# Kernel optimization log

Measured on AMD Instinct MI355X. Metric: run time of the kernel, lower is better.

Reference implementation:

```python
import jax, jax.numpy as jnp
import numpy as np

B, S, D = 2, 2048, 1024
H, HD = 16, 64  # n_heads, head_dim


def setup_inputs() -> dict:
    key = jax.random.key(0)
    ks = jax.random.split(key, 6)
    scale = 1.0 / np.sqrt(D)
    return {
        "Q": jax.random.normal(ks[0], (B, S, D), dtype=jnp.float32),
        "K": jax.random.normal(ks[1], (B, S, D), dtype=jnp.float32),
        "V": jax.random.normal(ks[2], (B, S, D), dtype=jnp.float32),
        "Wq": jax.random.normal(ks[3], (H, D, HD), dtype=jnp.float32) * scale,
        "Wv": jax.random.normal(ks[4], (H, D, HD), dtype=jnp.float32) * scale,
        "Wo": jax.random.normal(ks[5], (D, D), dtype=jnp.float32) * scale,
        "bo": jnp.zeros((D,), dtype=jnp.float32),
    }


def reference(Q, K, V, Wq, Wv, Wo, bo):
    # NOTE: original code projects K with the *query* weight (bug kept for fidelity).
    q = jnp.einsum("bsd,hdk->bhsk", Q, Wq)   # [B,H,S,HD]
    k = jnp.einsum("bsd,hdk->bhsk", K, Wq)   # query weights, per original
    v = jnp.einsum("bsd,hdk->bhsk", V, Wv)
    scores = jnp.einsum("bhsk,bhtk->bhst", q, k) / jnp.sqrt(jnp.asarray(HD, q.dtype))
    weights = jax.nn.softmax(scores, axis=-1)  # [B,H,S,S]
    attn = jnp.einsum("bhst,bhtk->bhsk", weights, v)  # [B,H,S,HD]
    concat = attn.transpose(0, 2, 1, 3).reshape(Q.shape[0], Q.shape[1], H * HD)
    return concat @ Wo.T + bo
```

## Files before the change

kernel.cpp:

```cpp
#include <hip/hip_runtime.h>

typedef __attribute__((ext_vector_type(8))) short short8;
typedef __attribute__((ext_vector_type(4))) short short4v;
typedef __attribute__((ext_vector_type(4))) float f32x4;
typedef __attribute__((ext_vector_type(16))) float f32x16;

__device__ __forceinline__ unsigned short f2bf(float f) {
  union { float f; unsigned u; } v; v.f = f;
  unsigned u = v.u;
  unsigned r = (u + 0x7FFFu + ((u >> 16) & 1u)) >> 16;
  return (unsigned short)r;
}

__device__ __forceinline__ unsigned cvtpk(float lo, float hi) {
  unsigned r;
  asm("v_cvt_pk_bf16_f32 %0, %1, %2" : "=v"(r) : "v"(lo), "v"(hi));
  return r;
}

#if __has_builtin(__builtin_amdgcn_exp2f)
__device__ __forceinline__ float exp2_fast(float x) { return __builtin_amdgcn_exp2f(x); }
#else
__device__ __forceinline__ float exp2_fast(float x) { return __expf(x * 0.69314718056f); }
#endif

__device__ __forceinline__ void gl16(const void* g, void* l) {
  __builtin_amdgcn_global_load_lds(
      (const __attribute__((address_space(1))) unsigned int*)g,
      (__attribute__((address_space(3))) unsigned int*)l, 16, 0, 0);
}

#define QSCALE 0.1803368801111f

__global__ __launch_bounds__(256)
void prep_k(const float* __restrict__ Wq, const float* __restrict__ Wv,
            const float* __restrict__ Wo, unsigned short* __restrict__ BqT,
            unsigned short* __restrict__ BvT, unsigned short* __restrict__ BoT) {
  __shared__ float tile[64 * 65];
  const int bidx = blockIdx.x;
  const int tid = threadIdx.x;
  if (bidx < 512) {
    const float* W = (bidx < 256) ? Wq : Wv;
    unsigned short* Bt = (bidx < 256) ? BqT : BvT;
    const int bb = bidx & 255;
    const int h  = bb >> 4;
    const int d0 = (bb & 15) * 64;
#pragma unroll
    for (int i = 0; i < 16; ++i) {
      int e = i * 256 + tid;
      int r = e >> 6, c = e & 63;
      tile[r * 65 + c] = W[(size_t)h * 65536 + (size_t)(d0 + r) * 64 + c];
    }
    __syncthreads();
#pragma unroll
    for (int i = 0; i < 16; ++i) {
      int e = i * 256 + tid;
      int jj = e >> 6, dd = e & 63;
      Bt[(size_t)(h * 64 + jj) * 1024 + d0 + dd] = f2bf(tile[dd * 65 + jj]);
    }
  } else {
    size_t t = (size_t)(bidx - 512) * 256 + tid;
    float4 f = *(const float4*)(Wo + t * 4);
    short4v v;
    v[0] = (short)f2bf(f.x); v[1] = (short)f2bf(f.y);
    v[2] = (short)f2bf(f.z); v[3] = (short)f2bf(f.w);
    *(short4v*)((short*)BoT + t * 4) = v;
  }
}

__global__ __launch_bounds__(256)
void conv3_k(const float* __restrict__ Q, const float* __restrict__ K,
             const float* __restrict__ V, unsigned short* __restrict__ dst) {
  const int bidx = blockIdx.x;
  const int sec = bidx >> 11;
  const float* src = (sec == 0) ? Q : (sec == 1) ? K : V;
  const float scale = (sec == 0) ? QSCALE : 1.0f;
  size_t t = (size_t)(bidx & 2047) * 256 + threadIdx.x;
  const float* s = src + t * 8;
  float4 f0 = *(const float4*)s;
  float4 f1 = *(const float4*)(s + 4);
  short8 v;
  v[0] = (short)f2bf(f0.x * scale); v[1] = (short)f2bf(f0.y * scale);
  v[2] = (short)f2bf(f0.z * scale); v[3] = (short)f2bf(f0.w * scale);
  v[4] = (short)f2bf(f1.x * scale); v[5] = (short)f2bf(f1.y * scale);
  v[6] = (short)f2bf(f1.z * scale); v[7] = (short)f2bf(f1.w * scale);
  *(short8*)(dst + (size_t)sec * 4194304 + t * 8) = v;
}

template<int EPI>
__global__ __launch_bounds__(256, 2)
void gemm3_k(const unsigned short* __restrict__ A, const unsigned short* __restrict__ Bt,
             void* __restrict__ Cp, const float* __restrict__ bias) {
  __shared__ __attribute__((aligned(16))) unsigned short As[2][64 * 64];
  __shared__ __attribute__((aligned(16))) unsigned short Bs[2][128 * 64];
  const int tid = threadIdx.x;
  const int l = tid & 63;
  const int w = tid >> 6;
  const int wr = w >> 1, wc = w & 1;
  const int lg = l >> 4, lc = l & 15;
  const int nwg = (int)gridDim.x;
  const int bid = blockIdx.x;
  const int swz = (bid & 7) * (nwg >> 3) + (bid >> 3);
  const int bm = swz >> 3, bn = swz & 7;

  const int sr = tid >> 3, ss = tid & 7;
  const unsigned short* Asrc = A  + (size_t)(bm * 64  + sr) * 1024 + ((ss ^ (sr & 7)) * 8);
  const unsigned short* Bsrc = Bt + (size_t)(bn * 128 + sr) * 1024 + ((ss ^ (sr & 7)) * 8);

  f32x4 acc[2][4] = {};

  auto stage = [&](int bufn, int k0) {
    char* ad = (char*)&As[bufn][0] + tid * 16;
    char* bd = (char*)&Bs[bufn][0] + tid * 16;
    gl16(Asrc + k0,          ad);
    gl16(Asrc + 32768 + k0,  ad + 4096);
    gl16(Bsrc + k0,          bd);
    gl16(Bsrc + 32768 + k0,  bd + 4096);
    gl16(Bsrc + 65536 + k0,  bd + 8192);
    gl16(Bsrc + 98304 + k0,  bd + 12288);
  };

  stage(0, 0);
  __syncthreads();

  int buf = 0;
  for (int it = 0; it < 16; ++it) {
    if (it < 15) stage(buf ^ 1, (it + 1) * 64);
    const unsigned short* Ac = &As[buf][0];
    const unsigned short* Bc = &Bs[buf][0];
    short8 af[2][2], bf[4][2];
#pragma unroll
    for (int mi = 0; mi < 2; ++mi)
#pragma unroll
      for (int ks = 0; ks < 2; ++ks)
        af[mi][ks] = *(const short8*)&Ac[(wr * 32 + mi * 16 + lc) * 64 + (((ks * 4 + lg) ^ (lc & 7)) * 8)];
#pragma unroll
    for (int ni = 0; ni < 4; ++ni)
#pragma unroll
      for (int ks = 0; ks < 2; ++ks)
        bf[ni][ks] = *(const short8*)&Bc[(wc * 64 + ni * 16 + lc) * 64 + (((ks * 4 + lg) ^ (lc & 7)) * 8)];
#pragma unroll
    for (int mi = 0; mi < 2; ++mi)
#pragma unroll
      for (int ni = 0; ni < 4; ++ni) {
        acc[mi][ni] = __builtin_amdgcn_mfma_f32_16x16x32_bf16(af[mi][0], bf[ni][0], acc[mi][ni], 0, 0, 0);
        acc[mi][ni] = __builtin_amdgcn_mfma_f32_16x16x32_bf16(af[mi][1], bf[ni][1], acc[mi][ni], 0, 0, 0);
      }
    __syncthreads();
    buf ^= 1;
  }

  const int m0 = bm * 64 + wr * 32 + lg * 4;
  const int n0 = bn * 128 + wc * 64 + lc;
#pragma unroll
  for (int mi = 0; mi < 2; ++mi) {
#pragma unroll
    for (int ni = 0; ni < 4; ++ni) {
      if (EPI == 1) {
        int m = m0 + mi * 16;
        int bb = m >> 11, s = m & 2047;
        int n = n0 + ni * 16;
        int hh = n >> 6, hd = n & 63;
        short4v pk;
#pragma unroll
        for (int j = 0; j < 4; ++j) pk[j] = (short)f2bf(acc[mi][ni][j]);
        *(short4v*)((unsigned short*)Cp + (size_t)((bb * 16 + hh) * 64 + hd) * 2048 + s) = pk;
      } else {
#pragma unroll
        for (int j = 0; j < 4; ++j) {
          int m = m0 + mi * 16 + j;
          int n = n0 + ni * 16;
          if (EPI == 2) ((float*)Cp)[(size_t)m * 1024 + n] = acc[mi][ni][j] + bias[n];
          else          ((unsigned short*)Cp)[(size_t)m * 1024 + n] = f2bf(acc[mi][ni][j]);
        }
      }
    }
  }
}

#define PACK8(SV, B0, W)                                                   \
  {                                                                        \
    float e0 = exp2_fast(SV[B0 + 0] - m_r), e1 = exp2_fast(SV[B0 + 1] - m_r); \
    float e2 = exp2_fast(SV[B0 + 2] - m_r), e3 = exp2_fast(SV[B0 + 3] - m_r); \
    float e4 = exp2_fast(SV[B0 + 4] - m_r), e5 = exp2_fast(SV[B0 + 5] - m_r); \
    float e6 = exp2_fast(SV[B0 + 6] - m_r), e7 = exp2_fast(SV[B0 + 7] - m_r); \
    l_r += ((e0 + e1) + (e2 + e3)) + ((e4 + e5) + (e6 + e7));              \
    unsigned Wa = cvtpk(e0, e1), Wb = cvtpk(e2, e3);                       \
    unsigned Wc = cvtpk(e4, e5), Wd = cvtpk(e6, e7);                       \
    unsigned pWa = __shfl_xor((int)Wa, 32), pWb = __shfl_xor((int)Wb, 32); \
    unsigned pWc = __shfl_xor((int)Wc, 32), pWd = __shfl_xor((int)Wd, 32); \
    W.x = hi ? pWc : Wa; W.y = hi ? pWd : Wb;                              \
    W.z = hi ? Wc : pWa; W.w = hi ? Wd : pWb;                              \
  }

#define MAX4(V, I) fmaxf(fmaxf(V[I], V[I + 1]), fmaxf(V[I + 2], V[I + 3]))

__global__ __launch_bounds__(256, 2)
void attn_k(const unsigned short* __restrict__ qh, const unsigned short* __restrict__ kh,
            const unsigned short* __restrict__ vT, unsigned short* __restrict__ attnc) {
  __shared__ __attribute__((aligned(16))) short Kb[2][4096];
  __shared__ __attribute__((aligned(16))) short Vb[2][4096];

  const int bid = (blockIdx.x & 7) * 64 + (blockIdx.x >> 3);
  const int qt = bid & 15;
  const int h = (bid >> 4) & 15;
  const int b = bid >> 8;
  const int tid = threadIdx.x;
  const int l = tid & 63;
  const int w = tid >> 6;
  const int q = l & 31;
  const int hi = l >> 5;
  const int ax = l & 7;

  const unsigned short* qb  = qh + (size_t)(b * 2048) * 1024 + h * 64;
  const unsigned short* kbf = kh + (size_t)(b * 2048) * 1024 + h * 64;
  const unsigned short* vb  = vT + (size_t)((b * 16 + h) * 64) * 2048;

  const int sr = tid >> 3, ss = tid & 7;
  const unsigned short* Ksrc = kbf + (size_t)sr * 1024 + ((ss ^ (sr & 7)) * 8);
  const unsigned short* Vsrc = vb  + (size_t)sr * 2048 + ((ss ^ (sr & 7)) * 8);

  const int s0 = qt * 128 + w * 32;
  short8 qf[4];
#pragma unroll
  for (int c = 0; c < 4; ++c)
    qf[c] = *(const short8*)(qb + (size_t)(s0 + q) * 1024 + c * 16 + hi * 8);

  float m_r = -1e30f, l_r = 0.f;
  f32x16 acc0 = {}, acc1 = {};
  const f32x16 zero16 = {};

  auto stageKV = [&](int bufn, int t0) {
    char* kd = (char*)&Kb[bufn][0] + tid * 16;
    char* vd = (char*)&Vb[bufn][0] + tid * 16;
    const unsigned short* ks = Ksrc + (size_t)t0 * 1024;
    const unsigned short* vs = Vsrc + t0;
    gl16(ks,         kd);
    gl16(ks + 32768, kd + 4096);
    gl16(vs,         vd);
    gl16(vs + 65536, vd + 4096);
  };

  stageKV(0, 0);
  __syncthreads();

  int cur = 0;
  for (int i = 0; i < 32; ++i) {
    if (i < 31) stageKV(cur ^ 1, (i + 1) * 64);

    const short* Kc = &Kb[cur][0];
    f32x16 sv0 = zero16, sv1 = zero16;
#pragma unroll
    for (int c = 0; c < 4; ++c) {
      const int gofs = (((c * 2 + hi) ^ ax) * 8);
      short8 kf0 = *(const short8*)&Kc[(q) * 64 + gofs];
      short8 kf1 = *(const short8*)&Kc[(32 + q) * 64 + gofs];
      sv0 = __builtin_amdgcn_mfma_f32_32x32x16_bf16(kf0, qf[c], sv0, 0, 0, 0);
      sv1 = __builtin_amdgcn_mfma_f32_32x32x16_bf16(kf1, qf[c], sv1, 0, 0, 0);
    }

    float tA = fmaxf(fmaxf(MAX4(sv0, 0), MAX4(sv0, 4)), fmaxf(MAX4(sv0, 8), MAX4(sv0, 12)));
    float tB = fmaxf(fmaxf(MAX4(sv1, 0), MAX4(sv1, 4)), fmaxf(MAX4(sv1, 8), MAX4(sv1, 12)));
    float tm = fmaxf(tA, tB);

    if (!__all(tm - m_r <= 8.0f)) {
      tm = fmaxf(tm, __shfl_xor(tm, 32));
      float mn = fmaxf(m_r, tm);
      float sc = exp2_fast(m_r - mn);
      m_r = mn;
      l_r *= sc;
#pragma unroll
      for (int j = 0; j < 16; ++j) { acc0[j] *= sc; acc1[j] *= sc; }
    }

    uint4 w0, w1, w2, w3;
    PACK8(sv0, 0, w0);
    PACK8(sv0, 8, w1);
    PACK8(sv1, 0, w2);
    PACK8(sv1, 8, w3);
    short8 pf0 = *reinterpret_cast<short8*>(&w0);
    short8 pf1 = *reinterpret_cast<short8*>(&w1);
    short8 pf2 = *reinterpret_cast<short8*>(&w2);
    short8 pf3 = *reinterpret_cast<short8*>(&w3);

    const short* Vc = &Vb[cur][0];
#pragma unroll
    for (int kc = 0; kc < 4; ++kc) {
      const int gofs = (((kc * 2 + hi) ^ ax) * 8);
      short8 vf0 = *(const short8*)&Vc[(q) * 64 + gofs];
      short8 vf1 = *(const short8*)&Vc[(32 + q) * 64 + gofs];
      short8 pf = (kc == 0) ? pf0 : (kc == 1) ? pf1 : (kc == 2) ? pf2 : pf3;
      acc0 = __builtin_amdgcn_mfma_f32_32x32x16_bf16(vf0, pf, acc0, 0, 0, 0);
      acc1 = __builtin_amdgcn_mfma_f32_32x32x16_bf16(vf1, pf, acc1, 0, 0, 0);
    }

    __syncthreads();
    cur ^= 1;
  }

  l_r += __shfl_xor(l_r, 32);
  float inv = 1.0f / l_r;

  unsigned short* outp = attnc + (size_t)(b * 2048 + s0 + q) * 1024 + h * 64;
#pragma unroll
  for (int t = 0; t < 4; ++t) {
    short4v p0, p1;
#pragma unroll
    for (int n = 0; n < 4; ++n) {
      p0[n] = (short)f2bf(acc0[t * 4 + n] * inv);
      p1[n] = (short)f2bf(acc1[t * 4 + n] * inv);
    }
    *(short4v*)(outp + (t * 8 + 4 * hi))      = p0;
    *(short4v*)(outp + (32 + t * 8 + 4 * hi)) = p1;
  }
}

extern "C" void kernel_launch(void* const* d_in, const int* in_sizes, int n_in,
                              void* d_out, int out_size, void* d_ws, size_t ws_size,
                              hipStream_t stream) {
  const float* Q  = (const float*)d_in[0];
  const float* Kt = (const float*)d_in[1];
  const float* V  = (const float*)d_in[2];
  const float* Wq = (const float*)d_in[3];
  const float* Wv = (const float*)d_in[4];
  const float* Wo = (const float*)d_in[5];
  const float* bo = (const float*)d_in[6];
  float* out = (float*)d_out;

  char* ws = (char*)d_ws;
  unsigned short* QKb  = (unsigned short*)(ws);
  unsigned short* Vb   = (unsigned short*)(ws + ((size_t)16 << 20));
  unsigned short* qh   = (unsigned short*)(ws + ((size_t)24 << 20));
  unsigned short* BqT  = (unsigned short*)(ws + ((size_t)40 << 20));
  unsigned short* BvT  = (unsigned short*)(ws + ((size_t)42 << 20));
  unsigned short* BoT  = (unsigned short*)(ws + ((size_t)44 << 20));
  unsigned short* vT   = QKb;
  unsigned short* attc = (unsigned short*)(ws + ((size_t)8 << 20));
  unsigned short* kh   = qh + (size_t)4096 * 1024;

  prep_k<<<1536, 256, 0, stream>>>(Wq, Wv, Wo, BqT, BvT, BoT);
  conv3_k<<<6144, 256, 0, stream>>>(Q, Kt, V, QKb);

  gemm3_k<0><<<1024, 256, 0, stream>>>(QKb, BqT, qh, nullptr);
  gemm3_k<1><<<512, 256, 0, stream>>>(Vb, BvT, vT, nullptr);

  attn_k<<<512, 256, 0, stream>>>(qh, kh, vT, attc);

  gemm3_k<2><<<512, 256, 0, stream>>>(attc, BoT, out, bo);
}
```

Measured before the change: 142.0 us.

## Split KV sequence across two wave groups per attention block and merge in LDS

The attention block grows from 256 to 512 threads. Two groups of four waves each process half of the 2048 keys for the same 128 queries, using separate double-buffered K/V regions in LDS. At the end, the second group writes its partial accumulators, running max and sum to LDS, and the first group combines them with a rescaled softmax merge before writing bf16 output. This halves the sequential KV loop per wave and doubles resident waves, aiming to hide latency. The cost is 64KB of LDS per block and a `launch_bounds(512,4)` hint that may squeeze registers and cause spills.

```diff
diff --git a/kernel.cpp b/kernel.cpp
--- a/kernel.cpp
+++ b/kernel.cpp
@@ -195,11 +195,10 @@
 
 #define MAX4(V, I) fmaxf(fmaxf(V[I], V[I + 1]), fmaxf(V[I + 2], V[I + 3]))
 
-__global__ __launch_bounds__(256, 2)
+__global__ __launch_bounds__(512, 4)
 void attn_k(const unsigned short* __restrict__ qh, const unsigned short* __restrict__ kh,
             const unsigned short* __restrict__ vT, unsigned short* __restrict__ attnc) {
-  __shared__ __attribute__((aligned(16))) short Kb[2][4096];
-  __shared__ __attribute__((aligned(16))) short Vb[2][4096];
+  __shared__ __attribute__((aligned(16))) short smem[32768];
 
   const int bid = (blockIdx.x & 7) * 64 + (blockIdx.x >> 3);
   const int qt = bid & 15;
@@ -208,6 +207,8 @@
   const int tid = threadIdx.x;
   const int l = tid & 63;
   const int w = tid >> 6;
+  const int g4 = w & 3;
+  const int hf = w >> 2;
   const int q = l & 31;
   const int hi = l >> 5;
   const int ax = l & 7;
@@ -216,11 +217,14 @@
   const unsigned short* kbf = kh + (size_t)(b * 2048) * 1024 + h * 64;
   const unsigned short* vb  = vT + (size_t)((b * 16 + h) * 64) * 2048;
 
-  const int sr = tid >> 3, ss = tid & 7;
-  const unsigned short* Ksrc = kbf + (size_t)sr * 1024 + ((ss ^ (sr & 7)) * 8);
-  const unsigned short* Vsrc = vb  + (size_t)sr * 2048 + ((ss ^ (sr & 7)) * 8);
-
-  const int s0 = qt * 128 + w * 32;
+  short* Kgrp = smem + hf * 16384;
+
+  const int t = tid & 255;
+  const int sr = t >> 3, ss = t & 7;
+  const unsigned short* Ksrc = kbf + (size_t)(hf * 1024 + sr) * 1024 + ((ss ^ (sr & 7)) * 8);
+  const unsigned short* Vsrc = vb + (size_t)sr * 2048 + hf * 1024 + ((ss ^ (sr & 7)) * 8);
+
+  const int s0 = qt * 128 + g4 * 32;
   short8 qf[4];
 #pragma unroll
   for (int c = 0; c < 4; ++c)
@@ -230,11 +234,11 @@
   f32x16 acc0 = {}, acc1 = {};
   const f32x16 zero16 = {};
 
-  auto stageKV = [&](int bufn, int t0) {
-    char* kd = (char*)&Kb[bufn][0] + tid * 16;
-    char* vd = (char*)&Vb[bufn][0] + tid * 16;
-    const unsigned short* ks = Ksrc + (size_t)t0 * 1024;
-    const unsigned short* vs = Vsrc + t0;
+  auto stageKV = [&](int bufn, int i) {
+    char* kd = (char*)(Kgrp + bufn * 4096) + t * 16;
+    char* vd = (char*)(Kgrp + 8192 + bufn * 4096) + t * 16;
+    const unsigned short* ks = Ksrc + (size_t)i * 65536;
+    const unsigned short* vs = Vsrc + i * 64;
     gl16(ks,         kd);
     gl16(ks + 32768, kd + 4096);
     gl16(vs,         vd);
@@ -245,10 +249,10 @@
   __syncthreads();
 
   int cur = 0;
-  for (int i = 0; i < 32; ++i) {
-    if (i < 31) stageKV(cur ^ 1, (i + 1) * 64);
-
-    const short* Kc = &Kb[cur][0];
+  for (int i = 0; i < 16; ++i) {
+    if (i < 15) stageKV(cur ^ 1, i + 1);
+
+    const short* Kc = Kgrp + cur * 4096;
     f32x16 sv0 = zero16, sv1 = zero16;
 #pragma unroll
     for (int c = 0; c < 4; ++c) {
@@ -283,7 +287,7 @@
     short8 pf2 = *reinterpret_cast<short8*>(&w2);
     short8 pf3 = *reinterpret_cast<short8*>(&w3);
 
-    const short* Vc = &Vb[cur][0];
+    const short* Vc = Kgrp + 8192 + cur * 4096;
 #pragma unroll
     for (int kc = 0; kc < 4; ++kc) {
       const int gofs = (((kc * 2 + hi) ^ ax) * 8);
@@ -299,19 +303,43 @@
   }
 
   l_r += __shfl_xor(l_r, 32);
-  float inv = 1.0f / l_r;
-
-  unsigned short* outp = attnc + (size_t)(b * 2048 + s0 + q) * 1024 + h * 64;
-#pragma unroll
-  for (int t = 0; t < 4; ++t) {
-    short4v p0, p1;
-#pragma unroll
-    for (int n = 0; n < 4; ++n) {
-      p0[n] = (short)f2bf(acc0[t * 4 + n] * inv);
-      p1[n] = (short)f2bf(acc1[t * 4 + n] * inv);
-    }
-    *(short4v*)(outp + (t * 8 + 4 * hi))      = p0;
-    *(short4v*)(outp + (32 + t * 8 + 4 * hi)) = p1;
+
+  float* C = (float*)smem;
+  if (hf == 1) {
+    float* c = C + (size_t)(tid - 256) * 36;
+    *(f32x4*)(c + 0)  = (f32x4){acc0[0], acc0[1], acc0[2], acc0[3]};
+    *(f32x4*)(c + 4)  = (f32x4){acc0[4], acc0[5], acc0[6], acc0[7]};
+    *(f32x4*)(c + 8)  = (f32x4){acc0[8], acc0[9], acc0[10], acc0[11]};
+    *(f32x4*)(c + 12) = (f32x4){acc0[12], acc0[13], acc0[14], acc0[15]};
+    *(f32x4*)(c + 16) = (f32x4){acc1[0], acc1[1], acc1[2], acc1[3]};
+    *(f32x4*)(c + 20) = (f32x4){acc1[4], acc1[5], acc1[6], acc1[7]};
+    *(f32x4*)(c + 24) = (f32x4){acc1[8], acc1[9], acc1[10], acc1[11]};
+    *(f32x4*)(c + 28) = (f32x4){acc1[12], acc1[13], acc1[14], acc1[15]};
+    c[32] = m_r;
+    c[33] = l_r;
+  }
+  __syncthreads();
+  if (hf == 0) {
+    const float* c = C + (size_t)tid * 36;
+    float m1 = c[32], l1 = c[33];
+    float mx = fmaxf(m_r, m1);
+    float ca = exp2_fast(m_r - mx);
+    float cb = exp2_fast(m1 - mx);
+    float inv = 1.0f / (l_r * ca + l1 * cb);
+    float fa = ca * inv, fb = cb * inv;
+
+    unsigned short* outp = attnc + (size_t)(b * 2048 + s0 + q) * 1024 + h * 64;
+#pragma unroll
+    for (int t4 = 0; t4 < 4; ++t4) {
+      short4v p0, p1;
+#pragma unroll
+      for (int n = 0; n < 4; ++n) {
+        p0[n] = (short)f2bf(acc0[t4 * 4 + n] * fa + c[t4 * 4 + n] * fb);
+        p1[n] = (short)f2bf(acc1[t4 * 4 + n] * fa + c[16 + t4 * 4 + n] * fb);
+      }
+      *(short4v*)(outp + (t4 * 8 + 4 * hi))      = p0;
+      *(short4v*)(outp + (32 + t4 * 8 + 4 * hi)) = p1;
+    }
   }
 }
 
@@ -344,7 +372,7 @@
   gemm3_k<0><<<1024, 256, 0, stream>>>(QKb, BqT, qh, nullptr);
   gemm3_k<1><<<512, 256, 0, stream>>>(Vb, BvT, vT, nullptr);
 
-  attn_k<<<512, 256, 0, stream>>>(qh, kh, vT, attc);
+  attn_k<<<512, 512, 0, stream>>>(qh, kh, vT, attc);
 
   gemm3_k<2><<<512, 256, 0, stream>>>(attc, BoT, out, bo);
 }
```

Measured after the change: 137.4 us. -3.2%, faster.
